# Optimization experiments

Hardware: AMD Instinct MI355X
Metric: run time of the kernel (lower is better)

## Reference

```python
import jax, jax.numpy as jnp
import numpy as np

S, B = 64, 16          # seq_len, batch
V = 32000              # ntoken
NINP = 512             # ninp (embedding / decoder input dim)
NHID = 1536            # nhid (intermediate LSTM layers)
NHL = 1024             # nhidlast (last LSTM layer)
E = 8                  # n_experts


def setup_inputs() -> dict:
    key = jax.random.key(0)
    ks = jax.random.split(key, 24)

    def unif(k, shape, r=0.1):
        return jax.random.uniform(k, shape, jnp.float32, -r, r)

    inp = {
        "tokens": jax.random.randint(ks[0], (S, B), 0, V),
        "h0": jnp.zeros((B, NHID), jnp.float32),
        "c0": jnp.zeros((B, NHID), jnp.float32),
        "h1": jnp.zeros((B, NHID), jnp.float32),
        "c1": jnp.zeros((B, NHID), jnp.float32),
        "h2": jnp.zeros((B, NHL), jnp.float32),
        "c2": jnp.zeros((B, NHL), jnp.float32),
        # parameters
        "emb": unif(ks[1], (V, NINP)),
        "Wih0": unif(ks[2], (4 * NHID, NINP)),
        "Whh0": unif(ks[3], (4 * NHID, NHID)),
        "b0": jnp.zeros((4 * NHID,), jnp.float32),
        "Wih1": unif(ks[4], (4 * NHID, NHID)),
        "Whh1": unif(ks[5], (4 * NHID, NHID)),
        "b1": jnp.zeros((4 * NHID,), jnp.float32),
        "Wih2": unif(ks[6], (4 * NHL, NHID)),
        "Whh2": unif(ks[7], (4 * NHL, NHL)),
        "b2": jnp.zeros((4 * NHL,), jnp.float32),
        "prior_W": unif(ks[8], (E, NHL)),
        "latent_W": unif(ks[9], (E * NINP, NHL)),
        "latent_b": jnp.zeros((E * NINP,), jnp.float32),
        "dec_W": unif(ks[10], (V, NINP)),
        "dec_b": jnp.zeros((V,), jnp.float32),
        "gain": jnp.ones((NINP,), jnp.float32),   # decoder_gain (frozen ones)
    }
    return inp


def _lstm_layer(x, h0, c0, Wih, Whh, b):
    # x: (S, B, Din); gate order i, f, g, o as in torch
    xg = jnp.einsum('sbd,gd->sbg', x, Wih) + b  # precompute input projections

    def step(carry, xt):
        h, c = carry
        g = xt + h @ Whh.T
        i, f, gg, o = jnp.split(g, 4, axis=-1)
        c = jax.nn.sigmoid(f) * c + jax.nn.sigmoid(i) * jnp.tanh(gg)
        h = jax.nn.sigmoid(o) * jnp.tanh(c)
        return (h, c), h

    (hT, cT), ys = jax.lax.scan(step, (h0, c0), xg)
    return ys, hT, cT


def reference(tokens, h0, c0, h1, c1, h2, c2, emb, Wih0, Whh0, b0,
              Wih1, Whh1, b1, Wih2, Whh2, b2, prior_W, latent_W, latent_b,
              dec_W, dec_b, gain):
    x = emb[tokens]                                   # (S, B, NINP)
    x, _, _ = _lstm_layer(x, h0, c0, Wih0, Whh0, b0)  # (S, B, NHID)
    x, _, _ = _lstm_layer(x, h1, c1, Wih1, Whh1, b1)  # (S, B, NHID)
    out, _, _ = _lstm_layer(x, h2, c2, Wih2, Whh2, b2)  # (S, B, NHL)

    # MoS head
    latent = jnp.tanh(jnp.einsum('sbh,eh->sbe', out, latent_W) + latent_b)
    latent = latent.reshape(S * B * E, NINP)          # (S*B*E, NINP)
    logit = (latent * gain) @ dec_W.T + dec_b         # (S*B*E, V)
    prior = jax.nn.softmax(out.reshape(S * B, NHL) @ prior_W.T, axis=-1)  # (S*B, E)
    prob = jax.nn.softmax(logit, axis=-1).reshape(S * B, E, V)
    prob = jnp.einsum('nev,ne->nv', prob, prior)      # mixture over experts
    log_prob = jnp.log(prob + 1e-8)
    return log_prob.reshape(S, B, V)
```

## Files before the change

kernel.cpp:

```cpp
#include <hip/hip_runtime.h>
#include <hip/hip_bf16.h>

typedef __attribute__((ext_vector_type(8))) short short8;
typedef __attribute__((ext_vector_type(4))) float f32x4;
typedef unsigned short u16;
typedef unsigned long long u64;

__device__ __forceinline__ u16 f2b(float f) {
    unsigned u = __float_as_uint(f);
    return (u16)((u + 0x7FFFu + ((u >> 16) & 1u)) >> 16);
}
__device__ __forceinline__ float b2f(u16 u) {
    return __uint_as_float(((unsigned)u) << 16);
}
__device__ __forceinline__ void gload16(const void* g, void* l) {
    __builtin_amdgcn_global_load_lds(
        (const __attribute__((address_space(1))) void*)g,
        (__attribute__((address_space(3))) void*)l, 16, 0, 0);
}

__global__ __launch_bounds__(256)
void k_f2b(const float* __restrict__ s, u16* __restrict__ d, int n4)
{
    int i = blockIdx.x * 256 + threadIdx.x;
    if (i >= n4) return;
    float4 v = ((const float4*)s)[i];
    short4 o;
    o.x = (short)f2b(v.x); o.y = (short)f2b(v.y);
    o.z = (short)f2b(v.z); o.w = (short)f2b(v.w);
    ((short4*)d)[i] = o;
}

__global__ __launch_bounds__(256)
void k_embed(const int* __restrict__ tok, const float* __restrict__ emb,
             u16* __restrict__ x0)
{
    int i = blockIdx.x * 256 + threadIdx.x;
    int n = i >> 7, p4 = i & 127;
    float4 v = ((const float4*)(emb + (size_t)tok[n] * 512))[p4];
    short4 o;
    o.x = (short)f2b(v.x); o.y = (short)f2b(v.y);
    o.z = (short)f2b(v.z); o.w = (short)f2b(v.w);
    ((short4*)x0)[i] = o;
}

template <int EPI, int BIN>
__global__ __launch_bounds__(256)
void k_gemm(const u16* __restrict__ A, const void* __restrict__ Bp,
            const float* __restrict__ bias, void* __restrict__ Cp,
            int M, int N, int K, const float* __restrict__ gain,
            float* __restrict__ rsum)
{
    __shared__ __align__(16) u16 As[128 * 32];
    __shared__ __align__(16) u16 Bs[128 * 32];
    __shared__ float rs[2][128];
    const int tid = threadIdx.x;
    const int lane = tid & 63, wid = tid >> 6;
    const int wr = wid >> 1, wc = wid & 1;
    const int l15 = lane & 15, l4 = lane >> 4;
    const int row0 = blockIdx.y * 128, col0 = blockIdx.x * 128;

    const int srA = wid * 16 + (lane >> 2);
    const int skA = (lane & 3) * 8;
    const int srow = tid >> 1, skh = (tid & 1) << 4;

    f32x4 acc[4][4] = {};

    for (int k0 = 0; k0 < K; k0 += 32) {
        if (k0) __syncthreads();
        gload16(A + (size_t)(row0 + srA) * K + k0 + skA, As + wid * 512);
        gload16(A + (size_t)(row0 + 64 + srA) * K + k0 + skA, As + 2048 + wid * 512);
        if (BIN == 1) {
            const u16* B = (const u16*)Bp;
            gload16(B + (size_t)(col0 + srA) * K + k0 + skA, Bs + wid * 512);
            gload16(B + (size_t)(col0 + 64 + srA) * K + k0 + skA, Bs + 2048 + wid * 512);
        } else {
            const float* B = (const float*)Bp;
            const float4* sb = (const float4*)(B + (size_t)(col0 + srow) * K + k0 + skh);
            float tmp[16];
            *(float4*)&tmp[0]  = sb[0];
            *(float4*)&tmp[4]  = sb[1];
            *(float4*)&tmp[8]  = sb[2];
            *(float4*)&tmp[12] = sb[3];
            short8 v0, v1;
#pragma unroll
            for (int i = 0; i < 8; ++i) { v0[i] = (short)f2b(tmp[i]); v1[i] = (short)f2b(tmp[8 + i]); }
            *(short8*)&Bs[srow * 32 + skh]     = v0;
            *(short8*)&Bs[srow * 32 + skh + 8] = v1;
        }
        __syncthreads();

        short8 af[4], bfv[4];
#pragma unroll
        for (int i = 0; i < 4; ++i)
            af[i]  = *(const short8*)&As[(wr * 64 + i * 16 + l15) * 32 + l4 * 8];
#pragma unroll
        for (int i = 0; i < 4; ++i)
            bfv[i] = *(const short8*)&Bs[(wc * 64 + i * 16 + l15) * 32 + l4 * 8];
#pragma unroll
        for (int mi = 0; mi < 4; ++mi)
#pragma unroll
            for (int ni = 0; ni < 4; ++ni)
                acc[mi][ni] = __builtin_amdgcn_mfma_f32_16x16x32_bf16(
                    af[mi], bfv[ni], acc[mi][ni], 0, 0, 0);
    }

    if (EPI == 2) {
#pragma unroll
        for (int mi = 0; mi < 4; ++mi) {
#pragma unroll
            for (int j = 0; j < 4; ++j) {
                int rb = row0 + wr * 64 + mi * 16 + l4 * 4 + j;
                float rsub = 0.f;
#pragma unroll
                for (int ni = 0; ni < 4; ++ni) {
                    int cc = col0 + wc * 64 + ni * 16 + l15;
                    float pv = expf(fminf(acc[mi][ni][j] + bias[cc], 80.f));
                    ((u16*)Cp)[(size_t)rb * N + cc] = f2b(pv);
                    rsub += pv;
                }
#pragma unroll
                for (int o = 1; o < 16; o <<= 1) rsub += __shfl_xor(rsub, o, 64);
                if (l15 == 0)
                    rs[wc][wr * 64 + mi * 16 + l4 * 4 + j] = rsub;
            }
        }
        __syncthreads();
        if (tid < 128)
            atomicAdd(&rsum[row0 + tid], rs[0][tid] + rs[1][tid]);
        return;
    }

#pragma unroll
    for (int mi = 0; mi < 4; ++mi) {
#pragma unroll
        for (int ni = 0; ni < 4; ++ni) {
            int rb = row0 + wr * 64 + mi * 16 + l4 * 4;
            int cc = col0 + wc * 64 + ni * 16 + l15;
            float bv = bias[cc];
#pragma unroll
            for (int j = 0; j < 4; ++j) {
                float v = acc[mi][ni][j] + bv;
                if (EPI == 0) {
                    ((float*)Cp)[(size_t)(rb + j) * N + cc] = v;
                } else {
                    int e = cc >> 9, pp = cc & 511;
                    ((u16*)Cp)[(((size_t)(rb + j) * 8 + e) << 9) | pp] =
                        f2b(tanhf(v) * gain[pp]);
                }
            }
        }
    }
}

__global__ __launch_bounds__(512)
void k_gemm_dec2(const u16* __restrict__ A, const u16* __restrict__ B,
                 const float* __restrict__ bias, u16* __restrict__ pe,
                 int M, int N, int K, float* __restrict__ rsum)
{
    __shared__ __align__(16) u16 As[256 * 32];
    __shared__ __align__(16) u16 Bs[256 * 32];
    __shared__ float rs[4][256];
    const int tid = threadIdx.x;
    const int lane = tid & 63, wid = tid >> 6;
    const int wr = wid >> 2, wc = wid & 3;
    const int l15 = lane & 15, l4 = lane >> 4;
    const int row0 = blockIdx.y * 256, col0 = blockIdx.x * 256;

    const int srA = wid * 16 + (lane >> 2);
    const int skA = (lane & 3) * 8;

    f32x4 acc[8][4] = {};

    for (int k0 = 0; k0 < K; k0 += 32) {
        if (k0) __syncthreads();
        gload16(A + (size_t)(row0 + srA) * K + k0 + skA, As + wid * 512);
        gload16(A + (size_t)(row0 + 128 + srA) * K + k0 + skA, As + 4096 + wid * 512);
        gload16(B + (size_t)(col0 + srA) * K + k0 + skA, Bs + wid * 512);
        gload16(B + (size_t)(col0 + 128 + srA) * K + k0 + skA, Bs + 4096 + wid * 512);
        __syncthreads();

        short8 af[8], bfv[4];
#pragma unroll
        for (int i = 0; i < 8; ++i)
            af[i]  = *(const short8*)&As[(wr * 128 + i * 16 + l15) * 32 + l4 * 8];
#pragma unroll
        for (int i = 0; i < 4; ++i)
            bfv[i] = *(const short8*)&Bs[(wc * 64 + i * 16 + l15) * 32 + l4 * 8];
#pragma unroll
        for (int mi = 0; mi < 8; ++mi)
#pragma unroll
            for (int ni = 0; ni < 4; ++ni)
                acc[mi][ni] = __builtin_amdgcn_mfma_f32_16x16x32_bf16(
                    af[mi], bfv[ni], acc[mi][ni], 0, 0, 0);
    }

#pragma unroll
    for (int mi = 0; mi < 8; ++mi) {
#pragma unroll
        for (int j = 0; j < 4; ++j) {
            int rloc = wr * 128 + mi * 16 + l4 * 4 + j;
            float rsub = 0.f;
#pragma unroll
            for (int ni = 0; ni < 4; ++ni) {
                int cc = col0 + wc * 64 + ni * 16 + l15;
                float pv = expf(fminf(acc[mi][ni][j] + bias[cc], 80.f));
                pe[(size_t)(row0 + rloc) * N + cc] = f2b(pv);
                rsub += pv;
            }
#pragma unroll
            for (int o = 1; o < 16; o <<= 1) rsub += __shfl_xor(rsub, o, 64);
            if (l15 == 0) rs[wc][rloc] = rsub;
        }
    }
    __syncthreads();
    if (tid < 256)
        atomicAdd(&rsum[row0 + tid],
                  rs[0][tid] + rs[1][tid] + rs[2][tid] + rs[3][tid]);
}

template <int DH>
__global__ void __launch_bounds__(512)
k_rnn(const float* __restrict__ xg,
      const u16* __restrict__ W,
      const float* __restrict__ h0f,
      const float* __restrict__ c0f,
      u16* __restrict__ y,
      unsigned* __restrict__ bar,
      int nb)
{
    constexpr int DH2 = DH / 2;
    constexpr int NSH = DH2 / 32;
    constexpr int NL  = 16 * DH / 4 / 512;
    constexpr int RW  = DH / 4;
    constexpr int LDH = DH + 8;
    __shared__ __align__(16) u16 hs[16][LDH];
    __shared__ __align__(16) f32x4 red[8][64];
    __shared__ __align__(16) u16 hout[16][16];

    const int tid = threadIdx.x;
    const int lane = tid & 63, wid = tid >> 6;
    const int g = wid & 3, kh = wid >> 2;
    const int l15 = lane & 15, l4 = lane >> 4;
    const int u0 = blockIdx.x * 16;

    short8 wfr[NSH];
    {
        const u16* wa = W + (size_t)(g * DH + u0 + l15) * DH + kh * DH2 + l4 * 8;
#pragma unroll
        for (int s = 0; s < NSH; ++s) wfr[s] = *(const short8*)(wa + s * 32);
    }

    const int eb = tid >> 4, eu = tid & 15;
    float c_reg = (tid < 256) ? c0f[(size_t)eb * DH + u0 + eu] : 0.f;

    for (int t = 0; t < 64; ++t) {
        float xpre[4];
        if (tid < 256) {
            const float* xr = xg + (size_t)(t * 16 + eb) * 4 * DH + u0 + eu;
#pragma unroll
            for (int gg = 0; gg < 4; ++gg) xpre[gg] = xr[(size_t)gg * DH];
        }

        if (t == 0) {
            for (int i = tid; i < 16 * DH / 4; i += 512) {
                int r = i / (DH / 4), k4 = i % (DH / 4);
                float4 v = *(const float4*)(h0f + (size_t)r * DH + k4 * 4);
                short4 o;
                o.x = (short)f2b(v.x); o.y = (short)f2b(v.y);
                o.z = (short)f2b(v.z); o.w = (short)f2b(v.w);
                *(short4*)&hs[r][k4 * 4] = o;
            }
            __syncthreads();
        } else {
            if (tid < nb) {
                while (__hip_atomic_load(bar + tid * 32, __ATOMIC_RELAXED,
                                         __HIP_MEMORY_SCOPE_AGENT) < (unsigned)t)
                    __builtin_amdgcn_s_sleep(1);
            }
            __syncthreads();
            const u64* hp = (const u64*)(y + (size_t)(t - 1) * 16 * DH);
            u64 tmp[NL];
#pragma unroll
            for (int j = 0; j < NL; ++j)
                tmp[j] = __hip_atomic_load(hp + tid + j * 512, __ATOMIC_RELAXED,
                                           __HIP_MEMORY_SCOPE_AGENT);
#pragma unroll
            for (int j = 0; j < NL; ++j) {
                int idx = tid + j * 512;
                int r = idx / RW, c = (idx % RW) * 4;
                *(u64*)&hs[r][c] = tmp[j];
            }
            __syncthreads();
        }

        f32x4 acc = {};
#pragma unroll
        for (int s = 0; s < NSH; ++s) {
            short8 hf = *(const short8*)&hs[l15][kh * DH2 + s * 32 + l4 * 8];
            acc = __builtin_amdgcn_mfma_f32_16x16x32_bf16(hf, wfr[s], acc, 0, 0, 0);
        }
        red[wid][lane] = acc;
        __syncthreads();

        if (tid < 256) {
            const int li = (eb >> 2) * 16 + eu, j = eb & 3;
            float gt[4];
#pragma unroll
            for (int gg = 0; gg < 4; ++gg)
                gt[gg] = ((const float*)&red[gg][li])[j]
                       + ((const float*)&red[4 + gg][li])[j]
                       + xpre[gg];
            float si = 1.f / (1.f + expf(-gt[0]));
            float sf = 1.f / (1.f + expf(-gt[1]));
            float so = 1.f / (1.f + expf(-gt[3]));
            c_reg = sf * c_reg + si * tanhf(gt[2]);
            hout[eb][eu] = f2b(so * tanhf(c_reg));
        }
        __syncthreads();

        if (tid < 64) {
            int r = tid >> 2, c4 = (tid & 3) * 4;
            u64 v = *(const u64*)&hout[r][c4];
            __hip_atomic_store((u64*)(y + (size_t)(t * 16 + r) * DH + u0 + c4), v,
                               __ATOMIC_RELAXED, __HIP_MEMORY_SCOPE_AGENT);
        }

        if (t < 63) {
            __syncthreads();
            if (tid == 0)
                __hip_atomic_store(bar + blockIdx.x * 32, (unsigned)(t + 1),
                                   __ATOMIC_RELAXED, __HIP_MEMORY_SCOPE_AGENT);
        }
    }
}

__global__ __launch_bounds__(256)
void k_prior(const u16* __restrict__ out2, const float* __restrict__ pW,
             float* __restrict__ prior)
{
    const int n = blockIdx.x;
    const int tid = threadIdx.x;
    const int e = tid >> 5, lane = tid & 31;
    const u16* x = out2 + (size_t)n * 1024;
    const float* w = pW + (size_t)e * 1024;
    float s = 0.f;
    for (int k = lane; k < 1024; k += 32) s += b2f(x[k]) * w[k];
#pragma unroll
    for (int o = 16; o; o >>= 1) s += __shfl_down(s, o, 32);
    __shared__ float es[8];
    if (lane == 0) es[e] = s;
    __syncthreads();
    if (tid == 0) {
        float m = -1e30f;
        for (int i = 0; i < 8; ++i) m = fmaxf(m, es[i]);
        float Z = 0.f, ex[8];
        for (int i = 0; i < 8; ++i) { ex[i] = expf(es[i] - m); Z += ex[i]; }
        for (int i = 0; i < 8; ++i) prior[(size_t)n * 8 + i] = ex[i] / Z;
    }
}

__global__ __launch_bounds__(128)
void k_combine(const u16* __restrict__ pe, const float* __restrict__ prior,
               const float* __restrict__ rsum, float* __restrict__ out, int n0)
{
    const int v2 = blockIdx.x * 128 + threadIdx.x;
    const int nl = blockIdx.y;
    __shared__ float w[8];
    if (threadIdx.x < 8)
        w[threadIdx.x] = prior[(size_t)(n0 + nl) * 8 + threadIdx.x]
                       / rsum[nl * 8 + threadIdx.x];
    __syncthreads();
    float a0 = 0.f, a1 = 0.f;
#pragma unroll
    for (int e = 0; e < 8; ++e) {
        unsigned pv = *(const unsigned*)&pe[(size_t)(nl * 8 + e) * 32000 + v2 * 2];
        a0 += b2f((u16)(pv & 0xffff)) * w[e];
        a1 += b2f((u16)(pv >> 16)) * w[e];
    }
    float2 o;
    o.x = logf(a0 + 1e-8f);
    o.y = logf(a1 + 1e-8f);
    *(float2*)&out[(size_t)(n0 + nl) * 32000 + v2 * 2] = o;
}

extern "C" void kernel_launch(void* const* d_in, const int* in_sizes, int n_in,
                              void* d_out, int out_size, void* d_ws, size_t ws_size,
                              hipStream_t stream)
{
    const int*   tok  = (const int*)d_in[0];
    const float* h0   = (const float*)d_in[1];
    const float* c0   = (const float*)d_in[2];
    const float* h1   = (const float*)d_in[3];
    const float* c1   = (const float*)d_in[4];
    const float* h2   = (const float*)d_in[5];
    const float* c2   = (const float*)d_in[6];
    const float* emb  = (const float*)d_in[7];
    const float* Wih0 = (const float*)d_in[8];
    const float* Whh0 = (const float*)d_in[9];
    const float* b0   = (const float*)d_in[10];
    const float* Wih1 = (const float*)d_in[11];
    const float* Whh1 = (const float*)d_in[12];
    const float* b1   = (const float*)d_in[13];
    const float* Wih2 = (const float*)d_in[14];
    const float* Whh2 = (const float*)d_in[15];
    const float* b2   = (const float*)d_in[16];
    const float* priW = (const float*)d_in[17];
    const float* latW = (const float*)d_in[18];
    const float* latb = (const float*)d_in[19];
    const float* decW = (const float*)d_in[20];
    const float* decb = (const float*)d_in[21];
    const float* gain = (const float*)d_in[22];

    char* p = (char*)d_ws;
    auto alloc = [&](size_t bytes) {
        char* r = p; p += (bytes + 255) & ~(size_t)255; return r;
    };
    u16* Whh0b = (u16*)alloc(6144ull * 1536 * 2);
    u16* Whh1b = (u16*)alloc(6144ull * 1536 * 2);
    u16* Whh2b = (u16*)alloc(4096ull * 1024 * 2);
    u16* latWb = (u16*)alloc(4096ull * 1024 * 2);
    u16* decWb = (u16*)alloc(32000ull * 512 * 2);
    u16* latb16 = (u16*)alloc(8192ull * 512 * 2);
    float* pri   = (float*)alloc(8192 * 4);
    float* rowsum = (float*)alloc(8192 * 4);
    u16* out2 = (u16*)alloc(1024ull * 1024 * 2);
    unsigned* bars = (unsigned*)alloc(3 * 96 * 32 * 4);
    char* trans = p;
    u16* Wih0b = (u16*)alloc(6144ull * 512 * 2);
    u16* Wih1b = (u16*)alloc(6144ull * 1536 * 2);
    u16* Wih2b = (u16*)alloc(4096ull * 1536 * 2);
    u16* x0 = (u16*)alloc(1024ull * 512 * 2);
    u16* x1 = (u16*)alloc(1024ull * 1536 * 2);
    u16* x2 = (u16*)alloc(1024ull * 1536 * 2);
    float* xg = (float*)alloc(1024ull * 6144 * 4);
    u16* pe = (u16*)trans;
    size_t cap = ws_size - (size_t)(trans - (char*)d_ws);
    int chunkRows = 128;
    if (cap >= 1024ull * 32000 * 2) chunkRows = 1024;
    else if (cap >= 512ull * 32000 * 2) chunkRows = 512;
    else if (cap >= 256ull * 32000 * 2) chunkRows = 256;
    int nPer = chunkRows / 8;

    hipMemsetAsync(bars, 0, 3 * 96 * 32 * 4, stream);
    hipMemsetAsync(rowsum, 0, 8192 * 4, stream);

    k_f2b<<<9216, 256, 0, stream>>>(Whh0, Whh0b, 2359296);
    k_f2b<<<9216, 256, 0, stream>>>(Whh1, Whh1b, 2359296);
    k_f2b<<<4096, 256, 0, stream>>>(Whh2, Whh2b, 1048576);
    k_f2b<<<3072, 256, 0, stream>>>(Wih0, Wih0b, 786432);
    k_f2b<<<9216, 256, 0, stream>>>(Wih1, Wih1b, 2359296);
    k_f2b<<<6144, 256, 0, stream>>>(Wih2, Wih2b, 1572864);
    k_f2b<<<4096, 256, 0, stream>>>(latW, latWb, 1048576);
    k_f2b<<<16000, 256, 0, stream>>>(decW, decWb, 4096000);
    k_embed<<<512, 256, 0, stream>>>(tok, emb, x0);

    k_gemm<0, 1><<<dim3(48, 8), 256, 0, stream>>>(
        x0, Wih0b, b0, xg, 1024, 6144, 512, nullptr, nullptr);
    {
        unsigned* bar = bars;
        int nb = 96;
        void* args[] = {(void*)&xg, (void*)&Whh0b, (void*)&h0, (void*)&c0,
                        (void*)&x1, (void*)&bar, (void*)&nb};
        hipLaunchCooperativeKernel(reinterpret_cast<void*>(&k_rnn<1536>),
                                   dim3(96), dim3(512), args, 0, stream);
    }

    k_gemm<0, 1><<<dim3(48, 8), 256, 0, stream>>>(
        x1, Wih1b, b1, xg, 1024, 6144, 1536, nullptr, nullptr);
    {
        unsigned* bar = bars + 96 * 32;
        int nb = 96;
        void* args[] = {(void*)&xg, (void*)&Whh1b, (void*)&h1, (void*)&c1,
                        (void*)&x2, (void*)&bar, (void*)&nb};
        hipLaunchCooperativeKernel(reinterpret_cast<void*>(&k_rnn<1536>),
                                   dim3(96), dim3(512), args, 0, stream);
    }

    k_gemm<0, 1><<<dim3(32, 8), 256, 0, stream>>>(
        x2, Wih2b, b2, xg, 1024, 4096, 1536, nullptr, nullptr);
    {
        unsigned* bar = bars + 2 * 96 * 32;
        int nb = 64;
        void* args[] = {(void*)&xg, (void*)&Whh2b, (void*)&h2, (void*)&c2,
                        (void*)&out2, (void*)&bar, (void*)&nb};
        hipLaunchCooperativeKernel(reinterpret_cast<void*>(&k_rnn<1024>),
                                   dim3(64), dim3(512), args, 0, stream);
    }

    k_prior<<<1024, 256, 0, stream>>>(out2, priW, pri);
    k_gemm<1, 1><<<dim3(32, 8), 256, 0, stream>>>(
        out2, latWb, latb, latb16, 1024, 4096, 1024, gain, nullptr);

    for (int nb = 0; nb < 1024; nb += nPer) {
        const u16* Ach = latb16 + (size_t)nb * 8 * 512;
        float* rsumc = rowsum + (size_t)nb * 8;
        if (chunkRows >= 256) {
            k_gemm_dec2<<<dim3(125, chunkRows / 256), 512, 0, stream>>>(
                Ach, decWb, decb, pe, chunkRows, 32000, 512, rsumc);
        } else {
            k_gemm<2, 1><<<dim3(250, chunkRows / 128), 256, 0, stream>>>(
                Ach, decWb, decb, pe, chunkRows, 32000, 512, nullptr, rsumc);
        }
        k_combine<<<dim3(125, nPer), 128, 0, stream>>>(
            pe, pri, rowsum + nb * 8, (float*)d_out, nb);
    }
}
```

Baseline: 1.560 ms.

## Overlap weight conversion with first LSTM, double-buffer GEMMs, retile decoder

Six of the fp32-to-bf16 weight conversions now run inside extra blocks of the first cooperative LSTM launch (grid grows from 96 to 256), so they overlap with the serial recurrence instead of running as separate kernels beforehand. Both GEMM kernels switch to double-buffered LDS staging, prefetching the next K slice while the MFMAs run on the current one and using one barrier per iteration. The decoder GEMM is retiled to 256x128 output tiles with 8 waves of 64x64, which halves per-block register accumulators and doubles the column-block count. The risk is that the extra conversion blocks compete with the recurrent blocks for memory bandwidth and compute units, and that the cooperative launch must keep all 256 blocks resident.

```diff
diff --git a/kernel.cpp b/kernel.cpp
--- a/kernel.cpp
+++ b/kernel.cpp
@@ -18,6 +18,13 @@
         (const __attribute__((address_space(1))) void*)g,
         (__attribute__((address_space(3))) void*)l, 16, 0, 0);
 }
+
+struct CvtJobs {
+    const float* s[6];
+    u16* d[6];
+    int n4[6];
+    int njobs;
+};
 
 __global__ __launch_bounds__(256)
 void k_f2b(const float* __restrict__ s, u16* __restrict__ d, int n4)
@@ -44,15 +51,15 @@
     ((short4*)x0)[i] = o;
 }
 
-template <int EPI, int BIN>
+template <int EPI>
 __global__ __launch_bounds__(256)
-void k_gemm(const u16* __restrict__ A, const void* __restrict__ Bp,
+void k_gemm(const u16* __restrict__ A, const u16* __restrict__ B,
             const float* __restrict__ bias, void* __restrict__ Cp,
             int M, int N, int K, const float* __restrict__ gain,
             float* __restrict__ rsum)
 {
-    __shared__ __align__(16) u16 As[128 * 32];
-    __shared__ __align__(16) u16 Bs[128 * 32];
+    __shared__ __align__(16) u16 As[2][128 * 32];
+    __shared__ __align__(16) u16 Bs[2][128 * 32];
     __shared__ float rs[2][128];
     const int tid = threadIdx.x;
     const int lane = tid & 63, wid = tid >> 6;
@@ -62,47 +69,37 @@
 
     const int srA = wid * 16 + (lane >> 2);
     const int skA = (lane & 3) * 8;
-    const int srow = tid >> 1, skh = (tid & 1) << 4;
+
+    auto stage = [&](int buf, int k0) {
+        gload16(A + (size_t)(row0 + srA) * K + k0 + skA, &As[buf][wid * 512]);
+        gload16(A + (size_t)(row0 + 64 + srA) * K + k0 + skA, &As[buf][2048 + wid * 512]);
+        gload16(B + (size_t)(col0 + srA) * K + k0 + skA, &Bs[buf][wid * 512]);
+        gload16(B + (size_t)(col0 + 64 + srA) * K + k0 + skA, &Bs[buf][2048 + wid * 512]);
+    };
 
     f32x4 acc[4][4] = {};
 
+    stage(0, 0);
+    __syncthreads();
+    int cur = 0;
     for (int k0 = 0; k0 < K; k0 += 32) {
-        if (k0) __syncthreads();
-        gload16(A + (size_t)(row0 + srA) * K + k0 + skA, As + wid * 512);
-        gload16(A + (size_t)(row0 + 64 + srA) * K + k0 + skA, As + 2048 + wid * 512);
-        if (BIN == 1) {
-            const u16* B = (const u16*)Bp;
-            gload16(B + (size_t)(col0 + srA) * K + k0 + skA, Bs + wid * 512);
-            gload16(B + (size_t)(col0 + 64 + srA) * K + k0 + skA, Bs + 2048 + wid * 512);
-        } else {
-            const float* B = (const float*)Bp;
-            const float4* sb = (const float4*)(B + (size_t)(col0 + srow) * K + k0 + skh);
-            float tmp[16];
-            *(float4*)&tmp[0]  = sb[0];
-            *(float4*)&tmp[4]  = sb[1];
-            *(float4*)&tmp[8]  = sb[2];
-            *(float4*)&tmp[12] = sb[3];
-            short8 v0, v1;
-#pragma unroll
-            for (int i = 0; i < 8; ++i) { v0[i] = (short)f2b(tmp[i]); v1[i] = (short)f2b(tmp[8 + i]); }
-            *(short8*)&Bs[srow * 32 + skh]     = v0;
-            *(short8*)&Bs[srow * 32 + skh + 8] = v1;
-        }
-        __syncthreads();
+        if (k0 + 32 < K) stage(cur ^ 1, k0 + 32);
 
         short8 af[4], bfv[4];
 #pragma unroll
         for (int i = 0; i < 4; ++i)
-            af[i]  = *(const short8*)&As[(wr * 64 + i * 16 + l15) * 32 + l4 * 8];
+            af[i]  = *(const short8*)&As[cur][(wr * 64 + i * 16 + l15) * 32 + l4 * 8];
 #pragma unroll
         for (int i = 0; i < 4; ++i)
-            bfv[i] = *(const short8*)&Bs[(wc * 64 + i * 16 + l15) * 32 + l4 * 8];
+            bfv[i] = *(const short8*)&Bs[cur][(wc * 64 + i * 16 + l15) * 32 + l4 * 8];
 #pragma unroll
         for (int mi = 0; mi < 4; ++mi)
 #pragma unroll
             for (int ni = 0; ni < 4; ++ni)
                 acc[mi][ni] = __builtin_amdgcn_mfma_f32_16x16x32_bf16(
                     af[mi], bfv[ni], acc[mi][ni], 0, 0, 0);
+        __syncthreads();
+        cur ^= 1;
     }
 
     if (EPI == 2) {
@@ -154,52 +151,58 @@
 }
 
 __global__ __launch_bounds__(512)
-void k_gemm_dec2(const u16* __restrict__ A, const u16* __restrict__ B,
-                 const float* __restrict__ bias, u16* __restrict__ pe,
-                 int M, int N, int K, float* __restrict__ rsum)
-{
-    __shared__ __align__(16) u16 As[256 * 32];
-    __shared__ __align__(16) u16 Bs[256 * 32];
-    __shared__ float rs[4][256];
+void k_gemm_dec(const u16* __restrict__ A, const u16* __restrict__ B,
+                const float* __restrict__ bias, u16* __restrict__ pe,
+                int M, int N, int K, float* __restrict__ rsum)
+{
+    __shared__ __align__(16) u16 As[2][256 * 32];
+    __shared__ __align__(16) u16 Bs[2][128 * 32];
+    __shared__ float rs[2][256];
     const int tid = threadIdx.x;
     const int lane = tid & 63, wid = tid >> 6;
-    const int wr = wid >> 2, wc = wid & 3;
+    const int wr = wid >> 1, wc = wid & 1;
     const int l15 = lane & 15, l4 = lane >> 4;
-    const int row0 = blockIdx.y * 256, col0 = blockIdx.x * 256;
+    const int row0 = blockIdx.y * 256, col0 = blockIdx.x * 128;
 
     const int srA = wid * 16 + (lane >> 2);
     const int skA = (lane & 3) * 8;
 
-    f32x4 acc[8][4] = {};
-
+    auto stage = [&](int buf, int k0) {
+        gload16(A + (size_t)(row0 + srA) * K + k0 + skA, &As[buf][wid * 512]);
+        gload16(A + (size_t)(row0 + 128 + srA) * K + k0 + skA, &As[buf][4096 + wid * 512]);
+        gload16(B + (size_t)(col0 + srA) * K + k0 + skA, &Bs[buf][wid * 512]);
+    };
+
+    f32x4 acc[4][4] = {};
+
+    stage(0, 0);
+    __syncthreads();
+    int cur = 0;
     for (int k0 = 0; k0 < K; k0 += 32) {
-        if (k0) __syncthreads();
-        gload16(A + (size_t)(row0 + srA) * K + k0 + skA, As + wid * 512);
-        gload16(A + (size_t)(row0 + 128 + srA) * K + k0 + skA, As + 4096 + wid * 512);
-        gload16(B + (size_t)(col0 + srA) * K + k0 + skA, Bs + wid * 512);
-        gload16(B + (size_t)(col0 + 128 + srA) * K + k0 + skA, Bs + 4096 + wid * 512);
-        __syncthreads();
-
-        short8 af[8], bfv[4];
-#pragma unroll
-        for (int i = 0; i < 8; ++i)
-            af[i]  = *(const short8*)&As[(wr * 128 + i * 16 + l15) * 32 + l4 * 8];
+        if (k0 + 32 < K) stage(cur ^ 1, k0 + 32);
+
+        short8 af[4], bfv[4];
 #pragma unroll
         for (int i = 0; i < 4; ++i)
-            bfv[i] = *(const short8*)&Bs[(wc * 64 + i * 16 + l15) * 32 + l4 * 8];
-#pragma unroll
-        for (int mi = 0; mi < 8; ++mi)
+            af[i]  = *(const short8*)&As[cur][(wr * 64 + i * 16 + l15) * 32 + l4 * 8];
+#pragma unroll
+        for (int i = 0; i < 4; ++i)
+            bfv[i] = *(const short8*)&Bs[cur][(wc * 64 + i * 16 + l15) * 32 + l4 * 8];
+#pragma unroll
+        for (int mi = 0; mi < 4; ++mi)
 #pragma unroll
             for (int ni = 0; ni < 4; ++ni)
                 acc[mi][ni] = __builtin_amdgcn_mfma_f32_16x16x32_bf16(
                     af[mi], bfv[ni], acc[mi][ni], 0, 0, 0);
-    }
-
-#pragma unroll
-    for (int mi = 0; mi < 8; ++mi) {
+        __syncthreads();
+        cur ^= 1;
+    }
+
+#pragma unroll
+    for (int mi = 0; mi < 4; ++mi) {
 #pragma unroll
         for (int j = 0; j < 4; ++j) {
-            int rloc = wr * 128 + mi * 16 + l4 * 4 + j;
+            int rloc = wr * 64 + mi * 16 + l4 * 4 + j;
             float rsub = 0.f;
 #pragma unroll
             for (int ni = 0; ni < 4; ++ni) {
@@ -215,8 +218,7 @@
     }
     __syncthreads();
     if (tid < 256)
-        atomicAdd(&rsum[row0 + tid],
-                  rs[0][tid] + rs[1][tid] + rs[2][tid] + rs[3][tid]);
+        atomicAdd(&rsum[row0 + tid], rs[0][tid] + rs[1][tid]);
 }
 
 template <int DH>
@@ -227,8 +229,25 @@
       const float* __restrict__ c0f,
       u16* __restrict__ y,
       unsigned* __restrict__ bar,
-      int nb)
-{
+      int nb, CvtJobs jobs)
+{
+    if ((int)blockIdx.x >= nb) {
+        const int hb = blockIdx.x - nb, nh = gridDim.x - nb;
+        for (int j = 0; j < jobs.njobs; ++j) {
+            const float4* s = (const float4*)jobs.s[j];
+            short4* d = (short4*)jobs.d[j];
+            const int n4 = jobs.n4[j];
+            for (int i = hb * 512 + threadIdx.x; i < n4; i += nh * 512) {
+                float4 v = s[i];
+                short4 o;
+                o.x = (short)f2b(v.x); o.y = (short)f2b(v.y);
+                o.z = (short)f2b(v.z); o.w = (short)f2b(v.w);
+                d[i] = o;
+            }
+        }
+        return;
+    }
+
     constexpr int DH2 = DH / 2;
     constexpr int NSH = DH2 / 32;
     constexpr int NL  = 16 * DH / 4 / 512;
@@ -446,60 +465,66 @@
     hipMemsetAsync(rowsum, 0, 8192 * 4, stream);
 
     k_f2b<<<9216, 256, 0, stream>>>(Whh0, Whh0b, 2359296);
-    k_f2b<<<9216, 256, 0, stream>>>(Whh1, Whh1b, 2359296);
-    k_f2b<<<4096, 256, 0, stream>>>(Whh2, Whh2b, 1048576);
     k_f2b<<<3072, 256, 0, stream>>>(Wih0, Wih0b, 786432);
-    k_f2b<<<9216, 256, 0, stream>>>(Wih1, Wih1b, 2359296);
-    k_f2b<<<6144, 256, 0, stream>>>(Wih2, Wih2b, 1572864);
-    k_f2b<<<4096, 256, 0, stream>>>(latW, latWb, 1048576);
-    k_f2b<<<16000, 256, 0, stream>>>(decW, decWb, 4096000);
     k_embed<<<512, 256, 0, stream>>>(tok, emb, x0);
 
-    k_gemm<0, 1><<<dim3(48, 8), 256, 0, stream>>>(
+    k_gemm<0><<<dim3(48, 8), 256, 0, stream>>>(
         x0, Wih0b, b0, xg, 1024, 6144, 512, nullptr, nullptr);
     {
         unsigned* bar = bars;
         int nb = 96;
+        CvtJobs jobs;
+        jobs.s[0] = Whh1; jobs.d[0] = Whh1b; jobs.n4[0] = 2359296;
+        jobs.s[1] = Whh2; jobs.d[1] = Whh2b; jobs.n4[1] = 1048576;
+        jobs.s[2] = Wih1; jobs.d[2] = Wih1b; jobs.n4[2] = 2359296;
+        jobs.s[3] = Wih2; jobs.d[3] = Wih2b; jobs.n4[3] = 1572864;
+        jobs.s[4] = latW; jobs.d[4] = latWb; jobs.n4[4] = 1048576;
+        jobs.s[5] = decW; jobs.d[5] = decWb; jobs.n4[5] = 4096000;
+        jobs.njobs = 6;
         void* args[] = {(void*)&xg, (void*)&Whh0b, (void*)&h0, (void*)&c0,
-                        (void*)&x1, (void*)&bar, (void*)&nb};
+                        (void*)&x1, (void*)&bar, (void*)&nb, (void*)&jobs};
         hipLaunchCooperativeKernel(reinterpret_cast<void*>(&k_rnn<1536>),
-                                   dim3(96), dim3(512), args, 0, stream);
-    }
-
-    k_gemm<0, 1><<<dim3(48, 8), 256, 0, stream>>>(
+                                   dim3(256), dim3(512), args, 0, stream);
+    }
+
+    k_gemm<0><<<dim3(48, 8), 256, 0, stream>>>(
         x1, Wih1b, b1, xg, 1024, 6144, 1536, nullptr, nullptr);
     {
         unsigned* bar = bars + 96 * 32;
         int nb = 96;
+        CvtJobs jobs;
+        jobs.njobs = 0;
         void* args[] = {(void*)&xg, (void*)&Whh1b, (void*)&h1, (void*)&c1,
-                        (void*)&x2, (void*)&bar, (void*)&nb};
+                        (void*)&x2, (void*)&bar, (void*)&nb, (void*)&jobs};
         hipLaunchCooperativeKernel(reinterpret_cast<void*>(&k_rnn<1536>),
                                    dim3(96), dim3(512), args, 0, stream);
     }
 
-    k_gemm<0, 1><<<dim3(32, 8), 256, 0, stream>>>(
+    k_gemm<0><<<dim3(32, 8), 256, 0, stream>>>(
         x2, Wih2b, b2, xg, 1024, 4096, 1536, nullptr, nullptr);
     {
         unsigned* bar = bars + 2 * 96 * 32;
         int nb = 64;
+        CvtJobs jobs;
+        jobs.njobs = 0;
         void* args[] = {(void*)&xg, (void*)&Whh2b, (void*)&h2, (void*)&c2,
-                        (void*)&out2, (void*)&bar, (void*)&nb};
+                        (void*)&out2, (void*)&bar, (void*)&nb, (void*)&jobs};
         hipLaunchCooperativeKernel(reinterpret_cast<void*>(&k_rnn<1024>),
                                    dim3(64), dim3(512), args, 0, stream);
     }
 
     k_prior<<<1024, 256, 0, stream>>>(out2, priW, pri);
-    k_gemm<1, 1><<<dim3(32, 8), 256, 0, stream>>>(
+    k_gemm<1><<<dim3(32, 8), 256, 0, stream>>>(
         out2, latWb, latb, latb16, 1024, 4096, 1024, gain, nullptr);
 
     for (int nb = 0; nb < 1024; nb += nPer) {
         const u16* Ach = latb16 + (size_t)nb * 8 * 512;
         float* rsumc = rowsum + (size_t)nb * 8;
         if (chunkRows >= 256) {
-            k_gemm_dec2<<<dim3(125, chunkRows / 256), 512, 0, stream>>>(
+            k_gemm_dec<<<dim3(250, chunkRows / 256), 512, 0, stream>>>(
                 Ach, decWb, decb, pe, chunkRows, 32000, 512, rsumc);
         } else {
-            k_gemm<2, 1><<<dim3(250, chunkRows / 128), 256, 0, stream>>>(
+            k_gemm<2><<<dim3(250, chunkRows / 128), 256, 0, stream>>>(
                 Ach, decWb, decb, pe, chunkRows, 32000, 512, nullptr, rsumc);
         }
         k_combine<<<dim3(125, nPer), 128, 0, stream>>>(
```

Measured after the change: 1.426 ms. -8.6%, faster.
